# Kernel optimization log

Hardware: AMD Instinct MI355X
Metric: run time of the kernel (lower is better)

## Reference

```python
import jax, jax.numpy as jnp
import numpy as np
import math

B, S, D, H = 2, 2048, 1024, 16
DQ = D // H  # d_qkv = 64


def setup_inputs() -> dict:
    key = jax.random.key(0)
    k1, k2, k3, k4 = jax.random.split(key, 4)
    return {
        "Q": jax.random.normal(k1, (B, S, D), dtype=jnp.float32),
        "K": jax.random.normal(k2, (B, S, D), dtype=jnp.float32),
        "V": jax.random.normal(k3, (B, S, D), dtype=jnp.float32),
        "Wo_w": jax.random.normal(k4, (D, D), dtype=jnp.float32) * 0.02,
        "Wo_b": jnp.zeros((D,), dtype=jnp.float32),
        "mask": 1,
    }


def reference(Q, K, V, Wo_w, Wo_b, mask):
    # Note: original module defines Wq/Wk/Wv but never applies them in forward.
    q = Q.reshape(B, S, H, DQ)
    k = K.reshape(B, S, H, DQ)
    v = V.reshape(B, S, H, DQ)
    # raw QK^T scores: [B, H, S, S]
    scores = jnp.einsum("bqhd,bkhd->bhqk", q, k)
    if mask:
        # torch.triu_indices(S, S) default offset=0 -> mask where key >= query
        # (diagonal included). Fill applied BEFORE the sqrt(d) scaling, as in source.
        tri = jnp.arange(S)[:, None] <= jnp.arange(S)[None, :]  # [S, S]
        scores = jnp.where(tri, jnp.float32(-1e9), scores)
    scale = scores / math.sqrt(DQ)
    attn = jax.nn.softmax(scale, axis=-1)
    ctx = jnp.einsum("bhqk,bkhd->bqhd", attn, v).reshape(B, S, D)
    return ctx @ Wo_w.T + Wo_b
```

## Files before the change

kernel.cpp:

```cpp
#include <hip/hip_runtime.h>
#include <hip/hip_bf16.h>
#include <stdint.h>

#define B_  2
#define S_  2048
#define D_  1024
#define H_  16
#define DQ_ 64
#define QT_ (S_/64)
#define FMAX_ 16.0f

typedef float f32x4 __attribute__((ext_vector_type(4)));
typedef short bf16x8 __attribute__((ext_vector_type(8)));

__device__ __forceinline__ unsigned short f2bf(float f) {
    uint32_t u = __float_as_uint(f);
    u += 0x7fffu + ((u >> 16) & 1u);
    return (unsigned short)(u >> 16);
}
__device__ __forceinline__ float bf2f(unsigned short u) {
    return __uint_as_float(((uint32_t)u) << 16);
}
__device__ __forceinline__ bf16x8 packbf8(float4 a, float4 b) {
    bf16x8 r;
    r[0]=(short)f2bf(a.x); r[1]=(short)f2bf(a.y);
    r[2]=(short)f2bf(a.z); r[3]=(short)f2bf(a.w);
    r[4]=(short)f2bf(b.x); r[5]=(short)f2bf(b.y);
    r[6]=(short)f2bf(b.z); r[7]=(short)f2bf(b.w);
    return r;
}

__global__ __launch_bounds__(256) void prep_kernel(
    const float* __restrict__ K, const float* __restrict__ V,
    const float* __restrict__ W,
    unsigned short* __restrict__ Kb, unsigned short* __restrict__ Vt,
    unsigned short* __restrict__ Wb, float* __restrict__ Pv)
{
    __shared__ unsigned short Ls[64][72];
    const int blk = blockIdx.x, tid = threadIdx.x;

    if (blk < 1024) {
        const int st = blk & 31, h = (blk >> 5) & 15, b = blk >> 9;
        {
            int row = tid >> 2, col0 = (tid & 3) * 16;
            const float* src = V + (((size_t)b*S_ + (size_t)st*64 + row)*D_ + h*64 + col0);
            float4 f0 = ((const float4*)src)[0];
            float4 f1 = ((const float4*)src)[1];
            float4 f2 = ((const float4*)src)[2];
            float4 f3 = ((const float4*)src)[3];
            unsigned short* d = &Ls[row][col0];
            d[0]=f2bf(f0.x); d[1]=f2bf(f0.y); d[2]=f2bf(f0.z); d[3]=f2bf(f0.w);
            d[4]=f2bf(f1.x); d[5]=f2bf(f1.y); d[6]=f2bf(f1.z); d[7]=f2bf(f1.w);
            d[8]=f2bf(f2.x); d[9]=f2bf(f2.y); d[10]=f2bf(f2.z); d[11]=f2bf(f2.w);
            d[12]=f2bf(f3.x); d[13]=f2bf(f3.y); d[14]=f2bf(f3.z); d[15]=f2bf(f3.w);
        }
        __syncthreads();
        {
            int d = tid >> 2, scol = (tid & 3) * 16;
            unsigned short tmp[16];
            float psum = 0.f;
            #pragma unroll
            for (int i = 0; i < 16; ++i) {
                unsigned short u = Ls[scol + i][d];
                tmp[i] = u;
                psum += bf2f(u);
            }
            unsigned short* dst = Vt + ((size_t)((b*H_ + h)*64 + d)*S_ + st*64 + scol);
            ((uint4*)dst)[0] = *((uint4*)tmp);
            ((uint4*)dst)[1] = *((uint4*)(tmp + 8));
            psum += __shfl_xor(psum, 1);
            psum += __shfl_xor(psum, 2);
            if ((tid & 3) == 0)
                Pv[((size_t)(b*H_ + h)*64 + d)*32 + st] = psum;
        }
    } else if (blk < 5120) {
        int i = (blk - 1024)*256 + tid;
        float4 f = ((const float4*)K)[i];
        ushort4 o;
        o.x = f2bf(f.x); o.y = f2bf(f.y); o.z = f2bf(f.z); o.w = f2bf(f.w);
        ((ushort4*)Kb)[i] = o;
    } else {
        int i = (blk - 5120)*256 + tid;
        float4 f = ((const float4*)W)[i];
        ushort4 o;
        o.x = f2bf(f.x); o.y = f2bf(f.y); o.z = f2bf(f.z); o.w = f2bf(f.w);
        ((ushort4*)Wb)[i] = o;
    }
}

__global__ __launch_bounds__(256, 2) void attn_kernel(
    const float* __restrict__ Q,
    const unsigned short* __restrict__ Kb,
    const unsigned short* __restrict__ Vtb,
    const float* __restrict__ Pv,
    unsigned short* __restrict__ ctx,
    const int* __restrict__ maskp)
{
    __shared__ unsigned short Ks [2][64][72];
    __shared__ unsigned short Vts[2][64][72];
    __shared__ unsigned short Ps [4][16][72];

    const int bid = blockIdx.x;
    const int g = bid & 31, pa = bid >> 5;
    const int h = g & 15, b = g >> 4;
    const int tid  = threadIdx.x;
    const int wave = tid >> 6, lane = tid & 63;
    const int quad = lane >> 4, ln = lane & 15;
    const int maskv = maskp[0];

    if (maskv && pa == 0 && tid < 64) {
        const float* p = Pv + ((size_t)(b*H_ + h)*64 + tid)*32;
        float s = 0.f;
        #pragma unroll
        for (int i = 0; i < 32; ++i) s += p[i];
        ctx[(size_t)b*S_*D_ + h*64 + tid] = f2bf(s * (1.0f/S_));
    }

    const int srow = tid >> 2, scol = (tid & 3)*16;
    const unsigned short* kbase =
        Kb + (((size_t)b*S_ + srow)*D_ + h*64 + scol);
    const unsigned short* vbase =
        Vtb + ((size_t)((b*H_ + h)*64 + srow)*S_ + scol);

    for (int t = 0; t < 2; ++t) {
        const int qt = t ? (QT_-1 - pa) : pa;
        const int niter = maskv ? (qt + 1) : QT_;

        const float* qrow =
            Q + (((size_t)b*S_ + (size_t)qt*64 + wave*16 + ln)*D_ + h*64);
        float4 q0 = ((const float4*)(qrow + quad*8))[0];
        float4 q1 = ((const float4*)(qrow + quad*8))[1];
        float4 q2 = ((const float4*)(qrow + 32 + quad*8))[0];
        float4 q3 = ((const float4*)(qrow + 32 + quad*8))[1];
        bf16x8 aq0 = packbf8(q0, q1);
        bf16x8 aq1 = packbf8(q2, q3);

        uint4 k0 = *((const uint4*)(kbase));
        uint4 k1 = *((const uint4*)(kbase + 8));
        uint4 v0 = *((const uint4*)(vbase));
        uint4 v1 = *((const uint4*)(vbase + 8));

        f32x4 o[4] = {};
        float l4[4] = {0.f, 0.f, 0.f, 0.f};
        const int qg = qt*64 + wave*16 + quad*4;

        if (t) __syncthreads();

        for (int j = 0; j < niter; ++j) {
            const int cur = j & 1;
            *((uint4*)&Ks [cur][srow][scol])   = k0;
            *((uint4*)&Ks [cur][srow][scol+8]) = k1;
            *((uint4*)&Vts[cur][srow][scol])   = v0;
            *((uint4*)&Vts[cur][srow][scol+8]) = v1;
            uint4 nk0, nk1, nv0, nv1;
            if (j + 1 < niter) {
                const unsigned short* kp = kbase + (size_t)(j+1)*64*D_;
                const unsigned short* vp = vbase + (j+1)*64;
                nk0 = *((const uint4*)(kp));
                nk1 = *((const uint4*)(kp + 8));
                nv0 = *((const uint4*)(vp));
                nv1 = *((const uint4*)(vp + 8));
            }
            __syncthreads();

            f32x4 s[4] = {};
            #pragma unroll
            for (int nt = 0; nt < 4; ++nt) {
                bf16x8 b0 = *(const bf16x8*)&Ks[cur][nt*16 + ln][quad*8];
                bf16x8 b1 = *(const bf16x8*)&Ks[cur][nt*16 + ln][32 + quad*8];
                s[nt] = __builtin_amdgcn_mfma_f32_16x16x32_bf16(aq0, b0, s[nt], 0,0,0);
                s[nt] = __builtin_amdgcn_mfma_f32_16x16x32_bf16(aq1, b1, s[nt], 0,0,0);
            }

            if (maskv && j == qt) {
                const int kg = j*64 + ln;
                #pragma unroll
                for (int nt = 0; nt < 4; ++nt)
                    #pragma unroll
                    for (int r = 0; r < 4; ++r) {
                        float e = ((kg + nt*16) >= (qg + r)) ? 0.0f
                                   : __expf(s[nt][r]*0.125f - FMAX_);
                        l4[r] += e;
                        Ps[wave][quad*4 + r][nt*16 + ln] = f2bf(e);
                    }
            } else {
                #pragma unroll
                for (int nt = 0; nt < 4; ++nt)
                    #pragma unroll
                    for (int r = 0; r < 4; ++r) {
                        float e = __expf(s[nt][r]*0.125f - FMAX_);
                        l4[r] += e;
                        Ps[wave][quad*4 + r][nt*16 + ln] = f2bf(e);
                    }
            }

            {
                bf16x8 a0 = *(const bf16x8*)&Ps[wave][ln][quad*8];
                bf16x8 a1 = *(const bf16x8*)&Ps[wave][ln][32 + quad*8];
                #pragma unroll
                for (int nt = 0; nt < 4; ++nt) {
                    bf16x8 b0 = *(const bf16x8*)&Vts[cur][nt*16 + ln][quad*8];
                    bf16x8 b1 = *(const bf16x8*)&Vts[cur][nt*16 + ln][32 + quad*8];
                    o[nt] = __builtin_amdgcn_mfma_f32_16x16x32_bf16(a0, b0, o[nt], 0,0,0);
                    o[nt] = __builtin_amdgcn_mfma_f32_16x16x32_bf16(a1, b1, o[nt], 0,0,0);
                }
            }
            k0 = nk0; k1 = nk1; v0 = nv0; v1 = nv1;
        }

        float inv[4];
        #pragma unroll
        for (int r = 0; r < 4; ++r) {
            float lr = l4[r];
            lr += __shfl_xor(lr, 1);
            lr += __shfl_xor(lr, 2);
            lr += __shfl_xor(lr, 4);
            lr += __shfl_xor(lr, 8);
            inv[r] = 1.0f / lr;
        }
        #pragma unroll
        for (int nt = 0; nt < 4; ++nt)
            #pragma unroll
            for (int r = 0; r < 4; ++r) {
                int q = qg + r;
                if (maskv && q == 0) continue;
                int c = h*64 + nt*16 + ln;
                ctx[((size_t)b*S_ + q)*D_ + c] = f2bf(o[nt][r]*inv[r]);
            }
        __syncthreads();
    }
}

__global__ __launch_bounds__(256, 2) void proj_kernel(
    const unsigned short* __restrict__ A,
    const unsigned short* __restrict__ Bw,
    const float* __restrict__ bias,
    float* __restrict__ out)
{
    __shared__ unsigned short As[2][64][72];
    __shared__ unsigned short Bs[2][128][72];
    const int nt0 = blockIdx.x;
    const int mt0 = blockIdx.y;
    const int tid  = threadIdx.x;
    const int wave = tid >> 6, lane = tid & 63;
    const int quad = lane >> 4, ln = lane & 15;

    const int arow = tid >> 2, acol = (tid & 3)*16;
    const int brow = tid >> 1, bcol = (tid & 1)*32;
    const unsigned short* aptr = A  + ((size_t)(mt0*64  + arow)*1024 + acol);
    const unsigned short* bptr = Bw + ((size_t)(nt0*128 + brow)*1024 + bcol);

    uint4 a0 = ((const uint4*)aptr)[0], a1 = ((const uint4*)aptr)[1];
    uint4 b0 = ((const uint4*)bptr)[0], b1 = ((const uint4*)bptr)[1],
          b2 = ((const uint4*)bptr)[2], b3 = ((const uint4*)bptr)[3];

    f32x4 acc[4][2] = {};

    for (int kt = 0; kt < 16; ++kt) {
        const int cur = kt & 1;
        *((uint4*)&As[cur][arow][acol])    = a0;
        *((uint4*)&As[cur][arow][acol+8])  = a1;
        *((uint4*)&Bs[cur][brow][bcol])    = b0;
        *((uint4*)&Bs[cur][brow][bcol+8])  = b1;
        *((uint4*)&Bs[cur][brow][bcol+16]) = b2;
        *((uint4*)&Bs[cur][brow][bcol+24]) = b3;
        uint4 na0, na1, nb0, nb1, nb2, nb3;
        if (kt < 15) {
            const unsigned short* ap = aptr + (kt+1)*64;
            const unsigned short* bp = bptr + (kt+1)*64;
            na0 = ((const uint4*)ap)[0]; na1 = ((const uint4*)ap)[1];
            nb0 = ((const uint4*)bp)[0]; nb1 = ((const uint4*)bp)[1];
            nb2 = ((const uint4*)bp)[2]; nb3 = ((const uint4*)bp)[3];
        }
        __syncthreads();
        #pragma unroll
        for (int ks = 0; ks < 2; ++ks) {
            bf16x8 am[4], bn[2];
            #pragma unroll
            for (int i = 0; i < 4; ++i)
                am[i] = *(const bf16x8*)&As[cur][i*16 + ln][ks*32 + quad*8];
            #pragma unroll
            for (int i = 0; i < 2; ++i)
                bn[i] = *(const bf16x8*)&Bs[cur][wave*32 + i*16 + ln][ks*32 + quad*8];
            #pragma unroll
            for (int mi = 0; mi < 4; ++mi)
                #pragma unroll
                for (int ni = 0; ni < 2; ++ni)
                    acc[mi][ni] = __builtin_amdgcn_mfma_f32_16x16x32_bf16(
                        am[mi], bn[ni], acc[mi][ni], 0,0,0);
        }
        a0 = na0; a1 = na1;
        b0 = nb0; b1 = nb1; b2 = nb2; b3 = nb3;
    }

    #pragma unroll
    for (int mi = 0; mi < 4; ++mi)
        #pragma unroll
        for (int ni = 0; ni < 2; ++ni) {
            int row = mt0*64 + mi*16 + quad*4;
            int col = nt0*128 + wave*32 + ni*16 + ln;
            float bv = bias[col];
            #pragma unroll
            for (int r = 0; r < 4; ++r)
                out[(size_t)(row + r)*1024 + col] = acc[mi][ni][r] + bv;
        }
}

extern "C" void kernel_launch(void* const* d_in, const int* in_sizes, int n_in,
                              void* d_out, int out_size, void* d_ws, size_t ws_size,
                              hipStream_t stream)
{
    const float* Q   = (const float*)d_in[0];
    const float* K   = (const float*)d_in[1];
    const float* V   = (const float*)d_in[2];
    const float* Wo  = (const float*)d_in[3];
    const float* Wb  = (const float*)d_in[4];
    const int* maskp = (const int*)d_in[5];
    float* out = (float*)d_out;

    unsigned short* Kb   = (unsigned short*)d_ws;
    unsigned short* Vtb  = Kb  + (size_t)B_*S_*D_;
    unsigned short* Wob  = Vtb + (size_t)B_*S_*D_;
    unsigned short* ctxb = Wob + (size_t)D_*D_;
    float* Pv = (float*)(ctxb + (size_t)B_*S_*D_);

    prep_kernel<<<6144, 256, 0, stream>>>(K, V, Wo, Kb, Vtb, Wob, Pv);
    attn_kernel<<<512, 256, 0, stream>>>(Q, Kb, Vtb, Pv, ctxb, maskp);
    proj_kernel<<<dim3(8, 64), 256, 0, stream>>>(ctxb, Wob, Wb, out);
}
```

Before: 154.2 us.

## Use two 32-query waves per block with transposed score MFMA and exp2 softmax

```diff
diff --git a/kernel.cpp b/kernel.cpp
--- a/kernel.cpp
+++ b/kernel.cpp
@@ -8,7 +8,8 @@
 #define H_  16
 #define DQ_ 64
 #define QT_ (S_/64)
-#define FMAX_ 16.0f
+#define EXPC1_ 0.18033688f
+#define EXPC2_ (-23.083121f)
 
 typedef float f32x4 __attribute__((ext_vector_type(4)));
 typedef short bf16x8 __attribute__((ext_vector_type(8)));
@@ -88,7 +89,7 @@
     }
 }
 
-__global__ __launch_bounds__(256, 2) void attn_kernel(
+__global__ __launch_bounds__(128, 2) void attn_kernel(
     const float* __restrict__ Q,
     const unsigned short* __restrict__ Kb,
     const unsigned short* __restrict__ Vtb,
@@ -98,7 +99,7 @@
 {
     __shared__ unsigned short Ks [2][64][72];
     __shared__ unsigned short Vts[2][64][72];
-    __shared__ unsigned short Ps [4][16][72];
+    __shared__ unsigned short Ps [2][32][72];
 
     const int bid = blockIdx.x;
     const int g = bid & 31, pa = bid >> 5;
@@ -116,117 +117,133 @@
         ctx[(size_t)b*S_*D_ + h*64 + tid] = f2bf(s * (1.0f/S_));
     }
 
-    const int srow = tid >> 2, scol = (tid & 3)*16;
+    const int srow = tid >> 1, scol = (tid & 1)*32;
     const unsigned short* kbase =
         Kb + (((size_t)b*S_ + srow)*D_ + h*64 + scol);
     const unsigned short* vbase =
         Vtb + ((size_t)((b*H_ + h)*64 + srow)*S_ + scol);
 
+    const int qloc = wave*32 + ln;
+
     for (int t = 0; t < 2; ++t) {
         const int qt = t ? (QT_-1 - pa) : pa;
         const int niter = maskv ? (qt + 1) : QT_;
 
-        const float* qrow =
-            Q + (((size_t)b*S_ + (size_t)qt*64 + wave*16 + ln)*D_ + h*64);
-        float4 q0 = ((const float4*)(qrow + quad*8))[0];
-        float4 q1 = ((const float4*)(qrow + quad*8))[1];
-        float4 q2 = ((const float4*)(qrow + 32 + quad*8))[0];
-        float4 q3 = ((const float4*)(qrow + 32 + quad*8))[1];
-        bf16x8 aq0 = packbf8(q0, q1);
-        bf16x8 aq1 = packbf8(q2, q3);
-
-        uint4 k0 = *((const uint4*)(kbase));
-        uint4 k1 = *((const uint4*)(kbase + 8));
-        uint4 v0 = *((const uint4*)(vbase));
-        uint4 v1 = *((const uint4*)(vbase + 8));
-
-        f32x4 o[4] = {};
-        float l4[4] = {0.f, 0.f, 0.f, 0.f};
-        const int qg = qt*64 + wave*16 + quad*4;
-
-        if (t) __syncthreads();
+        bf16x8 bq[2][2];
+        #pragma unroll
+        for (int qt2 = 0; qt2 < 2; ++qt2) {
+            const float* qr = Q + (((size_t)b*S_ + (size_t)qt*64 + wave*32 + qt2*16 + ln)*D_
+                                   + h*64 + quad*8);
+            #pragma unroll
+            for (int dqs = 0; dqs < 2; ++dqs) {
+                float4 f0 = ((const float4*)(qr + dqs*32))[0];
+                float4 f1 = ((const float4*)(qr + dqs*32))[1];
+                bq[qt2][dqs] = packbf8(f0, f1);
+            }
+        }
+
+        uint4 kr[4], vr[4];
+        #pragma unroll
+        for (int u = 0; u < 4; ++u) {
+            kr[u] = ((const uint4*)kbase)[u];
+            vr[u] = ((const uint4*)vbase)[u];
+        }
+
+        f32x4 o[2][4] = {};
+        float l4[2] = {0.f, 0.f};
+        const int qg0 = qt*64 + wave*32;
 
         for (int j = 0; j < niter; ++j) {
             const int cur = j & 1;
-            *((uint4*)&Ks [cur][srow][scol])   = k0;
-            *((uint4*)&Ks [cur][srow][scol+8]) = k1;
-            *((uint4*)&Vts[cur][srow][scol])   = v0;
-            *((uint4*)&Vts[cur][srow][scol+8]) = v1;
-            uint4 nk0, nk1, nv0, nv1;
+            #pragma unroll
+            for (int u = 0; u < 4; ++u) {
+                *((uint4*)&Ks [cur][srow][scol + u*8]) = kr[u];
+                *((uint4*)&Vts[cur][srow][scol + u*8]) = vr[u];
+            }
             if (j + 1 < niter) {
                 const unsigned short* kp = kbase + (size_t)(j+1)*64*D_;
                 const unsigned short* vp = vbase + (j+1)*64;
-                nk0 = *((const uint4*)(kp));
-                nk1 = *((const uint4*)(kp + 8));
-                nv0 = *((const uint4*)(vp));
-                nv1 = *((const uint4*)(vp + 8));
+                #pragma unroll
+                for (int u = 0; u < 4; ++u) {
+                    kr[u] = ((const uint4*)kp)[u];
+                    vr[u] = ((const uint4*)vp)[u];
+                }
             }
             __syncthreads();
 
-            f32x4 s[4] = {};
-            #pragma unroll
-            for (int nt = 0; nt < 4; ++nt) {
-                bf16x8 b0 = *(const bf16x8*)&Ks[cur][nt*16 + ln][quad*8];
-                bf16x8 b1 = *(const bf16x8*)&Ks[cur][nt*16 + ln][32 + quad*8];
-                s[nt] = __builtin_amdgcn_mfma_f32_16x16x32_bf16(aq0, b0, s[nt], 0,0,0);
-                s[nt] = __builtin_amdgcn_mfma_f32_16x16x32_bf16(aq1, b1, s[nt], 0,0,0);
-            }
-
-            if (maskv && j == qt) {
-                const int kg = j*64 + ln;
-                #pragma unroll
-                for (int nt = 0; nt < 4; ++nt)
+            f32x4 s[4][2] = {};
+            #pragma unroll
+            for (int dqs = 0; dqs < 2; ++dqs)
+                #pragma unroll
+                for (int kt = 0; kt < 4; ++kt) {
+                    bf16x8 aK = *(const bf16x8*)&Ks[cur][kt*16 + ln][dqs*32 + quad*8];
+                    #pragma unroll
+                    for (int qt2 = 0; qt2 < 2; ++qt2)
+                        s[kt][qt2] = __builtin_amdgcn_mfma_f32_16x16x32_bf16(
+                            aK, bq[qt2][dqs], s[kt][qt2], 0,0,0);
+                }
+
+            const int diag = maskv && (j == qt);
+            #pragma unroll
+            for (int qt2 = 0; qt2 < 2; ++qt2) {
+                const int ql = qloc + qt2*16;
+                #pragma unroll
+                for (int kt = 0; kt < 4; ++kt) {
+                    float e[4];
                     #pragma unroll
                     for (int r = 0; r < 4; ++r) {
-                        float e = ((kg + nt*16) >= (qg + r)) ? 0.0f
-                                   : __expf(s[nt][r]*0.125f - FMAX_);
-                        l4[r] += e;
-                        Ps[wave][quad*4 + r][nt*16 + ln] = f2bf(e);
+                        float v = exp2f(fmaf(s[kt][qt2][r], EXPC1_, EXPC2_));
+                        if (diag && (kt*16 + quad*4 + r) >= ql) v = 0.f;
+                        e[r] = v;
                     }
-            } else {
-                #pragma unroll
-                for (int nt = 0; nt < 4; ++nt)
+                    l4[qt2] += (e[0] + e[1]) + (e[2] + e[3]);
+                    uint2 w;
+                    w.x = ((uint32_t)f2bf(e[1]) << 16) | f2bf(e[0]);
+                    w.y = ((uint32_t)f2bf(e[3]) << 16) | f2bf(e[2]);
+                    *((uint2*)&Ps[wave][qt2*16 + ln][kt*16 + quad*4]) = w;
+                }
+            }
+
+            bf16x8 ap[2][2];
+            #pragma unroll
+            for (int qt2 = 0; qt2 < 2; ++qt2)
+                #pragma unroll
+                for (int ks2 = 0; ks2 < 2; ++ks2)
+                    ap[qt2][ks2] = *(const bf16x8*)&Ps[wave][qt2*16 + ln][ks2*32 + quad*8];
+            #pragma unroll
+            for (int ks2 = 0; ks2 < 2; ++ks2)
+                #pragma unroll
+                for (int dd = 0; dd < 4; ++dd) {
+                    bf16x8 bv = *(const bf16x8*)&Vts[cur][dd*16 + ln][ks2*32 + quad*8];
                     #pragma unroll
-                    for (int r = 0; r < 4; ++r) {
-                        float e = __expf(s[nt][r]*0.125f - FMAX_);
-                        l4[r] += e;
-                        Ps[wave][quad*4 + r][nt*16 + ln] = f2bf(e);
-                    }
-            }
-
-            {
-                bf16x8 a0 = *(const bf16x8*)&Ps[wave][ln][quad*8];
-                bf16x8 a1 = *(const bf16x8*)&Ps[wave][ln][32 + quad*8];
-                #pragma unroll
-                for (int nt = 0; nt < 4; ++nt) {
-                    bf16x8 b0 = *(const bf16x8*)&Vts[cur][nt*16 + ln][quad*8];
-                    bf16x8 b1 = *(const bf16x8*)&Vts[cur][nt*16 + ln][32 + quad*8];
-                    o[nt] = __builtin_amdgcn_mfma_f32_16x16x32_bf16(a0, b0, o[nt], 0,0,0);
-                    o[nt] = __builtin_amdgcn_mfma_f32_16x16x32_bf16(a1, b1, o[nt], 0,0,0);
-                }
-            }
-            k0 = nk0; k1 = nk1; v0 = nv0; v1 = nv1;
-        }
-
-        float inv[4];
-        #pragma unroll
-        for (int r = 0; r < 4; ++r) {
-            float lr = l4[r];
-            lr += __shfl_xor(lr, 1);
-            lr += __shfl_xor(lr, 2);
-            lr += __shfl_xor(lr, 4);
-            lr += __shfl_xor(lr, 8);
-            inv[r] = 1.0f / lr;
-        }
-        #pragma unroll
-        for (int nt = 0; nt < 4; ++nt)
-            #pragma unroll
-            for (int r = 0; r < 4; ++r) {
-                int q = qg + r;
-                if (maskv && q == 0) continue;
-                int c = h*64 + nt*16 + ln;
-                ctx[((size_t)b*S_ + q)*D_ + c] = f2bf(o[nt][r]*inv[r]);
-            }
+                    for (int qt2 = 0; qt2 < 2; ++qt2)
+                        o[qt2][dd] = __builtin_amdgcn_mfma_f32_16x16x32_bf16(
+                            ap[qt2][ks2], bv, o[qt2][dd], 0,0,0);
+                }
+        }
+
+        #pragma unroll
+        for (int qt2 = 0; qt2 < 2; ++qt2) {
+            l4[qt2] += __shfl_xor(l4[qt2], 16);
+            l4[qt2] += __shfl_xor(l4[qt2], 32);
+        }
+        float inv[2][4];
+        #pragma unroll
+        for (int qt2 = 0; qt2 < 2; ++qt2)
+            #pragma unroll
+            for (int r = 0; r < 4; ++r)
+                inv[qt2][r] = 1.0f / __shfl(l4[qt2], quad*4 + r);
+        #pragma unroll
+        for (int qt2 = 0; qt2 < 2; ++qt2)
+            #pragma unroll
+            for (int dd = 0; dd < 4; ++dd)
+                #pragma unroll
+                for (int r = 0; r < 4; ++r) {
+                    int q = qg0 + qt2*16 + quad*4 + r;
+                    if (maskv && q == 0) continue;
+                    int c = h*64 + dd*16 + ln;
+                    ctx[((size_t)b*S_ + q)*D_ + c] = f2bf(o[qt2][dd][r]*inv[qt2][r]);
+                }
         __syncthreads();
     }
 }
@@ -325,6 +342,6 @@
     float* Pv = (float*)(ctxb + (size_t)B_*S_*D_);
 
     prep_kernel<<<6144, 256, 0, stream>>>(K, V, Wo, Kb, Vtb, Wob, Pv);
-    attn_kernel<<<512, 256, 0, stream>>>(Q, Kb, Vtb, Pv, ctxb, maskp);
+    attn_kernel<<<512, 128, 0, stream>>>(Q, Kb, Vtb, Pv, ctxb, maskp);
     proj_kernel<<<dim3(8, 64), 256, 0, stream>>>(ctxb, Wob, Wb, out);
 }
```

After: 214.3 us. +39.0%, slower.
